# Performance work log

Hardware: AMD Instinct MI355X
Metric: run time of the kernel (lower is better)

Reference implementation:

```python
import jax, jax.numpy as jnp
import numpy as np

B, T1, T2, D = 4, 128, 128, 300


def setup_inputs() -> dict:
    key = jax.random.key(0)
    ks = jax.random.split(key, 9)
    s = 1.0 / np.sqrt(D)
    return {
        "query": jax.random.normal(ks[0], (B, T1, D), jnp.float32),
        "key": jax.random.normal(ks[1], (B, T2, D), jnp.float32),
        "value": jax.random.normal(ks[2], (B, T2, D), jnp.float32),
        "hL": jax.random.normal(ks[3], (B, T1, T2, D), jnp.float32),
        "hR": jax.random.normal(ks[4], (B, T2, T1, D), jnp.float32),
        "WQ": jax.random.uniform(ks[5], (D, D), jnp.float32, -s, s),
        "bQ": jax.random.uniform(ks[6], (D,), jnp.float32, -s, s),
        "WK": jax.random.uniform(ks[7], (D, D), jnp.float32, -s, s),
        "bK": jax.random.uniform(ks[8], (D,), jnp.float32, -s, s),
    }


def reference(query, key, value, hL, hR, WQ, bQ, WK, bK):
    # Linear projections (torch nn.Linear: x @ W.T + b). Note fwK is applied
    # to BOTH key and value in the original module.
    q = query @ WQ.T + bQ            # [B, T1, D]
    k = key @ WK.T + bK              # [B, T2, D]
    v = value @ WK.T + bK            # [B, T2, D]

    hR_t = jnp.swapaxes(hR, 1, 2)    # [B, T1, T2, D]

    # concept-augmented scores: (q_i + hL_ij) . (k_j + hR_ji)
    q_plus_hL = q[:, :, None, :] + hL          # [B, T1, T2, D]
    k_plus_hR = k[:, None, :, :] + hR_t        # [B, T1, T2, D]
    scores = jnp.einsum("bijd,bijd->bij", q_plus_hL, k_plus_hR)  # [B, T1, T2]

    p_attn = jax.nn.softmax(scores, axis=-1)   # [B, T1, T2] (dropout p=0.0)

    # sharpening=True path: re-softmax with temperature 1/1000 then clamp
    attn = jnp.clip(jax.nn.softmax(1000.0 * p_attn, axis=-1), 0.0, 1.0)

    v_aug = v[:, None, :, :] + hR_t            # [B, T1, T2, D]
    x = jnp.einsum("bij,bijd->bid", attn, v_aug)  # [B, T1, D]
    return x
```

## Files before the change

### kernel.cpp

```cpp
#include <hip/hip_runtime.h>

#define BB 4
#define T 128
#define D 300
#define D4 75
#define NROW 512


__global__ __launch_bounds__(320) void proj_kernel(
    const float* __restrict__ query, const float* __restrict__ key,
    const float* __restrict__ value,
    const float* __restrict__ WQ, const float* __restrict__ bQ,
    const float* __restrict__ WK, const float* __restrict__ bK,
    float* __restrict__ qkv )
{
    const int src  = blockIdx.x >> 6;
    const int rblk = blockIdx.x & 63;
    const int r0   = rblk * 8;
    const float* in   = (src == 0) ? query : (src == 1 ? key : value);
    const float* W    = (src == 0) ? WQ : WK;
    const float* bias = (src == 0) ? bQ : bK;
    float* out = qkv + src * (NROW * D);

    __shared__ __align__(16) float lds_in[8 * D];
    for (int idx = threadIdx.x; idx < 8 * D; idx += 320)
        lds_in[idx] = in[r0 * D + idx];
    __syncthreads();

    const int t = threadIdx.x;
    if (t < D) {
        float acc[8];
        const float bv = bias[t];
        #pragma unroll
        for (int r = 0; r < 8; ++r) acc[r] = bv;
        const float4* W4 = (const float4*)(W + t * D);
        for (int e4 = 0; e4 < D4; ++e4) {
            const float4 w = W4[e4];
            #pragma unroll
            for (int r = 0; r < 8; ++r) {
                const float4 x = *(const float4*)(&lds_in[r * D + e4 * 4]);
                acc[r] += w.x * x.x + w.y * x.y + w.z * x.z + w.w * x.w;
            }
        }
        #pragma unroll
        for (int r = 0; r < 8; ++r)
            out[(r0 + r) * D + t] = acc[r];
    }
}

__global__ __launch_bounds__(1024) void attn_kernel(
    const float* __restrict__ hL, const float* __restrict__ hR,
    const float* __restrict__ qkv, float* __restrict__ outp)
{
    const int b = blockIdx.x >> 7;
    const int i = blockIdx.x & 127;

    const float* qp    = qkv + (b * T + i) * D;
    const float* kbase = qkv + NROW * D + b * T * D;
    const float* vbase = qkv + 2 * NROW * D + b * T * D;

    __shared__ __align__(16) float q_lds[D];
    __shared__ float sc[T];
    __shared__ __align__(16) float red[12][D];

    for (int idx = threadIdx.x; idx < D; idx += 1024) q_lds[idx] = qp[idx];
    __syncthreads();

    const int wave = threadIdx.x >> 6;
    const int lane = threadIdx.x & 63;

    const float4* hL4 = (const float4*)(hL + (size_t)(b * T + i) * T * D);
    for (int j = wave; j < T; j += 16) {
        const float4* hRrow = (const float4*)(hR + ((size_t)(b * T + j) * T + i) * D);
        const float4* krow  = (const float4*)(kbase + j * D);
        float4 a = {0.f, 0.f, 0.f, 0.f};
        #pragma unroll
        for (int it = 0; it < 2; ++it) {
            const int d4 = lane + it * 64;
            if (d4 < D4) {
                const float4 l  = hL4[j * D4 + d4];
                const float4 r  = hRrow[d4];
                const float4 kk = krow[d4];
                const float4 qq = *(const float4*)(&q_lds[d4 * 4]);
                a.x += (qq.x + l.x) * (kk.x + r.x);
                a.y += (qq.y + l.y) * (kk.y + r.y);
                a.z += (qq.z + l.z) * (kk.z + r.z);
                a.w += (qq.w + l.w) * (kk.w + r.w);
            }
        }
        float s = a.x + a.y + a.z + a.w;
        #pragma unroll
        for (int off = 32; off > 0; off >>= 1)
            s += __shfl_down(s, off, 64);
        if (lane == 0) sc[j] = s;
    }
    __syncthreads();

    if (wave == 0) {
        float s0 = sc[lane], s1 = sc[lane + 64];
        float m = fmaxf(s0, s1);
        #pragma unroll
        for (int off = 32; off > 0; off >>= 1) m = fmaxf(m, __shfl_xor(m, off, 64));
        float e0 = __expf(s0 - m), e1 = __expf(s1 - m);
        float sum = e0 + e1;
        #pragma unroll
        for (int off = 32; off > 0; off >>= 1) sum += __shfl_xor(sum, off, 64);
        const float inv = 1.0f / sum;
        float t0 = 1000.0f * (e0 * inv), t1 = 1000.0f * (e1 * inv);
        float m2 = fmaxf(t0, t1);
        #pragma unroll
        for (int off = 32; off > 0; off >>= 1) m2 = fmaxf(m2, __shfl_xor(m2, off, 64));
        float f0 = __expf(t0 - m2), f1 = __expf(t1 - m2);
        float sum2 = f0 + f1;
        #pragma unroll
        for (int off = 32; off > 0; off >>= 1) sum2 += __shfl_xor(sum2, off, 64);
        const float inv2 = 1.0f / sum2;
        sc[lane]      = fminf(fmaxf(f0 * inv2, 0.f), 1.f);
        sc[lane + 64] = fminf(fmaxf(f1 * inv2, 0.f), 1.f);
    }
    __syncthreads();

    const int tid = threadIdx.x;
    if (tid < 12 * D4) {
        const int grp = tid / D4;
        const int d4  = tid % D4;
        float4 acc = {0.f, 0.f, 0.f, 0.f};
        for (int j = grp; j < T; j += 12) {
            const float aj = sc[j];
            if (aj >= 1e-12f) {
                const float4 v4 = *(const float4*)(vbase + j * D + d4 * 4);
                const float4 r4 = *(const float4*)(hR + ((size_t)(b * T + j) * T + i) * D + d4 * 4);
                acc.x += aj * (v4.x + r4.x);
                acc.y += aj * (v4.y + r4.y);
                acc.z += aj * (v4.z + r4.z);
                acc.w += aj * (v4.w + r4.w);
            }
        }
        *(float4*)(&red[grp][d4 * 4]) = acc;
    }
    __syncthreads();
    if (tid < D4) {
        float4 o = {0.f, 0.f, 0.f, 0.f};
        #pragma unroll
        for (int g = 0; g < 12; ++g) {
            const float4 p = *(const float4*)(&red[g][tid * 4]);
            o.x += p.x; o.y += p.y; o.z += p.z; o.w += p.w;
        }
        *(float4*)(outp + (size_t)(b * T + i) * D + tid * 4) = o;
    }
}

extern "C" void kernel_launch(void* const* d_in, const int* in_sizes, int n_in,
                              void* d_out, int out_size, void* d_ws, size_t ws_size,
                              hipStream_t stream) {
    const float* query = (const float*)d_in[0];
    const float* key   = (const float*)d_in[1];
    const float* value = (const float*)d_in[2];
    const float* hL    = (const float*)d_in[3];
    const float* hR    = (const float*)d_in[4];
    const float* WQ    = (const float*)d_in[5];
    const float* bQ    = (const float*)d_in[6];
    const float* WK    = (const float*)d_in[7];
    const float* bK    = (const float*)d_in[8];
    float* out = (float*)d_out;
    float* qkv = (float*)d_ws;

    proj_kernel<<<dim3(192), dim3(320), 0, stream>>>(query, key, value, WQ, bQ, WK, bK, qkv);
    attn_kernel<<<dim3(512), dim3(1024), 0, stream>>>(hL, hR, qkv, out);
}
```

Before: 227.3 us.

## Process four query rows per block with LDS-staged hR tiles and swizzled grid

The attention kernel now handles 4 consecutive query rows per 512-thread block instead of one row per 1024-thread block. For each j-tile of 8 keys it stages the contiguous 4-row hR slab and the K rows in LDS, so hR reads are larger and coalesced rather than 1200-byte strided fragments. Block indices are swizzled to spread batches across XCDs. The grid shrinks to 128 blocks, which may underfill a 256-CU GPU. The second hR pass in the value reduction still reads from global memory, and it adds 16 barriers per block.

```diff
diff --git a/kernel.cpp b/kernel.cpp
--- a/kernel.cpp
+++ b/kernel.cpp
@@ -48,56 +48,80 @@
     }
 }
 
-__global__ __launch_bounds__(1024) void attn_kernel(
+__global__ __launch_bounds__(512) void attn3_kernel(
     const float* __restrict__ hL, const float* __restrict__ hR,
     const float* __restrict__ qkv, float* __restrict__ outp)
 {
-    const int b = blockIdx.x >> 7;
-    const int i = blockIdx.x & 127;
+    const int swz = (blockIdx.x & 7) * 16 + (blockIdx.x >> 3);
+    const int b  = swz >> 5;
+    const int it = swz & 31;
+    const int i0 = it * 4;
 
-    const float* qp    = qkv + (b * T + i) * D;
-    const float* kbase = qkv + NROW * D + b * T * D;
-    const float* vbase = qkv + 2 * NROW * D + b * T * D;
+    __shared__ __align__(16) float4 hR_l[2400];
+    __shared__ __align__(16) float4 k_l[600];
+    __shared__ __align__(16) float4 q_l[300];
+    __shared__ float sc[4][T];
 
-    __shared__ __align__(16) float q_lds[D];
-    __shared__ float sc[T];
-    __shared__ __align__(16) float red[12][D];
+    const float4* hR4  = (const float4*)hR;
+    const float4* hL4  = (const float4*)hL;
+    const float4* qkv4 = (const float4*)qkv;
 
-    for (int idx = threadIdx.x; idx < D; idx += 1024) q_lds[idx] = qp[idx];
-    __syncthreads();
+    for (int idx = threadIdx.x; idx < 300; idx += 512)
+        q_l[idx] = qkv4[(size_t)(b * T + i0) * D4 + idx];
 
-    const int wave = threadIdx.x >> 6;
+    const int w    = threadIdx.x >> 6;
     const int lane = threadIdx.x & 63;
+    const int iw   = w & 3;
+    const int jh   = w >> 2;
+    const int i    = i0 + iw;
 
-    const float4* hL4 = (const float4*)(hL + (size_t)(b * T + i) * T * D);
-    for (int j = wave; j < T; j += 16) {
-        const float4* hRrow = (const float4*)(hR + ((size_t)(b * T + j) * T + i) * D);
-        const float4* krow  = (const float4*)(kbase + j * D);
-        float4 a = {0.f, 0.f, 0.f, 0.f};
+    for (int jt = 0; jt < 16; ++jt) {
+        const int j0 = jt * 8;
+        for (int idx = threadIdx.x; idx < 2400; idx += 512) {
+            const int g = idx / 300, off = idx - g * 300;
+            hR_l[idx] = hR4[((size_t)(b * T + j0 + g) * T + i0) * D4 + off];
+        }
+        for (int idx = threadIdx.x; idx < 600; idx += 512)
+            k_l[idx] = qkv4[(size_t)NROW * D4 + (size_t)(b * T + j0) * D4 + idx];
+        __syncthreads();
+
+        const float4* hLw = hL4 + ((size_t)(b * T + i) * T + j0 + jh * 4) * D4;
+        float a0 = 0.f, a1 = 0.f, a2 = 0.f, a3 = 0.f;
         #pragma unroll
-        for (int it = 0; it < 2; ++it) {
-            const int d4 = lane + it * 64;
-            if (d4 < D4) {
-                const float4 l  = hL4[j * D4 + d4];
-                const float4 r  = hRrow[d4];
-                const float4 kk = krow[d4];
-                const float4 qq = *(const float4*)(&q_lds[d4 * 4]);
-                a.x += (qq.x + l.x) * (kk.x + r.x);
-                a.y += (qq.y + l.y) * (kk.y + r.y);
-                a.z += (qq.z + l.z) * (kk.z + r.z);
-                a.w += (qq.w + l.w) * (kk.w + r.w);
+        for (int itr = 0; itr < 5; ++itr) {
+            const int c = itr * 64 + lane;
+            if (c < 4 * D4) {
+                const int jl = c / D4, d4 = c - jl * D4;
+                const int jg = jh * 4 + jl;
+                const float4 hl = hLw[c];
+                const float4 qq = q_l[iw * D4 + d4];
+                const float4 kk = k_l[jg * D4 + d4];
+                const float4 rr = hR_l[(jg * 4 + iw) * D4 + d4];
+                const float s = (qq.x + hl.x) * (kk.x + rr.x)
+                              + (qq.y + hl.y) * (kk.y + rr.y)
+                              + (qq.z + hl.z) * (kk.z + rr.z)
+                              + (qq.w + hl.w) * (kk.w + rr.w);
+                a0 += (jl == 0) ? s : 0.f;
+                a1 += (jl == 1) ? s : 0.f;
+                a2 += (jl == 2) ? s : 0.f;
+                a3 += (jl == 3) ? s : 0.f;
             }
         }
-        float s = a.x + a.y + a.z + a.w;
         #pragma unroll
-        for (int off = 32; off > 0; off >>= 1)
-            s += __shfl_down(s, off, 64);
-        if (lane == 0) sc[j] = s;
+        for (int off = 32; off > 0; off >>= 1) a0 += __shfl_xor(a0, off, 64);
+        #pragma unroll
+        for (int off = 32; off > 0; off >>= 1) a1 += __shfl_xor(a1, off, 64);
+        #pragma unroll
+        for (int off = 32; off > 0; off >>= 1) a2 += __shfl_xor(a2, off, 64);
+        #pragma unroll
+        for (int off = 32; off > 0; off >>= 1) a3 += __shfl_xor(a3, off, 64);
+        if (lane == 0)
+            *(float4*)(&sc[iw][j0 + jh * 4]) = make_float4(a0, a1, a2, a3);
+        __syncthreads();
     }
-    __syncthreads();
 
-    if (wave == 0) {
-        float s0 = sc[lane], s1 = sc[lane + 64];
+    if (w < 4) {
+        float s0 = sc[w][lane], s1 = sc[w][lane + 64];
         float m = fmaxf(s0, s1);
         #pragma unroll
         for (int off = 32; off > 0; off >>= 1) m = fmaxf(m, __shfl_xor(m, off, 64));
@@ -115,38 +139,30 @@
         #pragma unroll
         for (int off = 32; off > 0; off >>= 1) sum2 += __shfl_xor(sum2, off, 64);
         const float inv2 = 1.0f / sum2;
-        sc[lane]      = fminf(fmaxf(f0 * inv2, 0.f), 1.f);
-        sc[lane + 64] = fminf(fmaxf(f1 * inv2, 0.f), 1.f);
+        sc[w][lane]      = fminf(fmaxf(f0 * inv2, 0.f), 1.f);
+        sc[w][lane + 64] = fminf(fmaxf(f1 * inv2, 0.f), 1.f);
     }
     __syncthreads();
 
-    const int tid = threadIdx.x;
-    if (tid < 12 * D4) {
-        const int grp = tid / D4;
-        const int d4  = tid % D4;
+    const int row = threadIdx.x >> 7;
+    const int r   = threadIdx.x & 127;
+    if (r < D4) {
+        const int d4 = r;
+        const int ir = i0 + row;
+        const float4* v4b = qkv4 + 2 * NROW * D4 + (size_t)(b * T) * D4;
         float4 acc = {0.f, 0.f, 0.f, 0.f};
-        for (int j = grp; j < T; j += 12) {
-            const float aj = sc[j];
+        for (int j = 0; j < T; ++j) {
+            const float aj = sc[row][j];
             if (aj >= 1e-12f) {
-                const float4 v4 = *(const float4*)(vbase + j * D + d4 * 4);
-                const float4 r4 = *(const float4*)(hR + ((size_t)(b * T + j) * T + i) * D + d4 * 4);
-                acc.x += aj * (v4.x + r4.x);
-                acc.y += aj * (v4.y + r4.y);
-                acc.z += aj * (v4.z + r4.z);
-                acc.w += aj * (v4.w + r4.w);
+                const float4 vv = v4b[j * D4 + d4];
+                const float4 rr = hR4[((size_t)(b * T + j) * T + ir) * D4 + d4];
+                acc.x += aj * (vv.x + rr.x);
+                acc.y += aj * (vv.y + rr.y);
+                acc.z += aj * (vv.z + rr.z);
+                acc.w += aj * (vv.w + rr.w);
             }
         }
-        *(float4*)(&red[grp][d4 * 4]) = acc;
-    }
-    __syncthreads();
-    if (tid < D4) {
-        float4 o = {0.f, 0.f, 0.f, 0.f};
-        #pragma unroll
-        for (int g = 0; g < 12; ++g) {
-            const float4 p = *(const float4*)(&red[g][tid * 4]);
-            o.x += p.x; o.y += p.y; o.z += p.z; o.w += p.w;
-        }
-        *(float4*)(outp + (size_t)(b * T + i) * D + tid * 4) = o;
+        ((float4*)outp)[(size_t)(b * T + ir) * D4 + d4] = acc;
     }
 }
 
@@ -166,5 +182,5 @@
     float* qkv = (float*)d_ws;
 
     proj_kernel<<<dim3(192), dim3(320), 0, stream>>>(query, key, value, WQ, bQ, WK, bK, qkv);
-    attn_kernel<<<dim3(512), dim3(1024), 0, stream>>>(hL, hR, qkv, out);
+    attn3_kernel<<<dim3(128), dim3(512), 0, stream>>>(hL, hR, qkv, out);
 }
```

Result: slower. 280.1 us (+23.2%).
